# Kernel optimization log

Hardware: AMD Instinct MI355X
Metric: run time of the kernel (lower is better)

Reference implementation:

```python
import jax, jax.numpy as jnp
import numpy as np

N_EMBD = 1024
N_HEAD = 16
HEAD_SIZE = N_EMBD // N_HEAD  # 64

def setup_inputs() -> dict:
    key = jax.random.key(0)
    ks = jax.random.split(key, 6)
    B, T, C, H, S = 2, 2048, N_EMBD, N_HEAD, HEAD_SIZE
    sc = 1.0 / np.sqrt(C)
    x = jax.random.normal(ks[0], (B, T, C), dtype=jnp.float32)
    # stacked per-head projection weights (no bias), [H, C, S]
    Wq = jax.random.normal(ks[1], (H, C, S), dtype=jnp.float32) * sc
    Wk = jax.random.normal(ks[2], (H, C, S), dtype=jnp.float32) * sc
    Wv = jax.random.normal(ks[3], (H, C, S), dtype=jnp.float32) * sc
    Wp = jax.random.normal(ks[4], (C, C), dtype=jnp.float32) * sc
    bp = jax.random.normal(ks[5], (C,), dtype=jnp.float32) * 0.01
    return {"x": x, "Wq": Wq, "Wk": Wk, "Wv": Wv, "Wp": Wp, "bp": bp}

def reference(x, Wq, Wk, Wv, Wp, bp):
    # Eval-mode forward (dropout = identity), default non-flash path.
    B, T, C = x.shape
    H, _, S = Wq.shape
    q = jnp.einsum('btc,hcs->bhts', x, Wq)
    k = jnp.einsum('btc,hcs->bhts', x, Wk)
    v = jnp.einsum('btc,hcs->bhts', x, Wv)
    att = jnp.einsum('bhts,bhus->bhtu', q, k) * (1.0 / np.sqrt(S))
    causal = jnp.tril(jnp.ones((T, T), dtype=bool))
    att = jnp.where(causal[None, None], att, -jnp.inf)
    att = jax.nn.softmax(att, axis=-1)
    y = jnp.einsum('bhtu,bhus->bhts', att, v)
    # concat heads along feature dim (head-major), then output projection
    y = y.transpose(0, 2, 1, 3).reshape(B, T, H * S)
    return y @ Wp.T + bp
```

## Files before the change

kernel.cpp:

```cpp
#include <hip/hip_runtime.h>
#include <hip/hip_bf16.h>
#include <cmath>

typedef __attribute__((ext_vector_type(8))) short bf16x8;
typedef __attribute__((ext_vector_type(4))) float f32x4;
typedef __attribute__((ext_vector_type(16))) float f32x16;

__device__ __forceinline__ unsigned short f2bf(float f) {
    union { float f; unsigned int i; } c; c.f = f;
    unsigned int i = c.i;
    unsigned int r = i + 0x7FFF + ((i >> 16) & 1);
    return (unsigned short)(r >> 16);
}

__device__ __forceinline__ float fast_exp2(float x) {
    float r;
    asm("v_exp_f32 %0, %1" : "=v"(r) : "v"(x));
    return r;
}

__device__ __forceinline__ void gload_lds16(const unsigned short* g, unsigned short* l) {
    __builtin_amdgcn_global_load_lds((const __attribute__((address_space(1))) unsigned int*)g,
                                     (__attribute__((address_space(3))) unsigned int*)l, 16, 0, 0);
}

__device__ __forceinline__ float bperm_f(int srclane, float v) {
    return __int_as_float(__builtin_amdgcn_ds_bpermute(srclane << 2, __float_as_int(v)));
}

__global__ void k_cvt(const float* __restrict__ src, unsigned short* __restrict__ dst, int n4) {
    int i = blockIdx.x * blockDim.x + threadIdx.x;
    if (i < n4) {
        float4 v = reinterpret_cast<const float4*>(src)[i];
        ushort4 o;
        o.x = f2bf(v.x); o.y = f2bf(v.y); o.z = f2bf(v.z); o.w = f2bf(v.w);
        reinterpret_cast<ushort4*>(dst)[i] = o;
    }
}

__global__ void k_cvt_wt(const float* __restrict__ Wq, const float* __restrict__ Wk,
                         const float* __restrict__ Wv, unsigned short* __restrict__ Wt) {
    __shared__ unsigned short lt[64][72];
    int bid = blockIdx.x;
    int ct  = bid & 15;
    int h   = (bid >> 4) & 15;
    int sec = bid >> 8;
    const float* W = (sec == 0) ? Wq : ((sec == 1) ? Wk : Wv);
    int t = threadIdx.x;
    #pragma unroll
    for (int q = 0; q < 4; q++) {
        int id = t + q * 256;
        int c  = id >> 4;
        int s4 = (id & 15) * 4;
        float4 v = *reinterpret_cast<const float4*>(&W[((size_t)(h * 1024) + (ct * 64 + c)) * 64 + s4]);
        lt[s4 + 0][c] = f2bf(v.x);
        lt[s4 + 1][c] = f2bf(v.y);
        lt[s4 + 2][c] = f2bf(v.z);
        lt[s4 + 3][c] = f2bf(v.w);
    }
    __syncthreads();
    #pragma unroll
    for (int q = 0; q < 2; q++) {
        int id = t + q * 256;
        int s  = id >> 3;
        int c8 = (id & 7) * 8;
        bf16x8 val = *reinterpret_cast<const bf16x8*>(&lt[s][c8]);
        int n = sec * 1024 + h * 64 + s;
        *reinterpret_cast<bf16x8*>(&Wt[(size_t)n * 1024 + ct * 64 + c8]) = val;
    }
}

template <int MODE>
__launch_bounds__(256)
__global__ void k_gemm(const unsigned short* __restrict__ A,
                       const unsigned short* __restrict__ Bt,
                       int M, int N, int K,
                       unsigned short* __restrict__ q_nat,
                       unsigned short* __restrict__ k_nat,
                       unsigned short* __restrict__ vT,
                       float* __restrict__ out, const float* __restrict__ bp) {
    __shared__ unsigned short Asm[128][64];
    __shared__ unsigned short Bsm[128][64];
    const int nb = N >> 7;
    int cpx = gridDim.x >> 3;
    int bid = (blockIdx.x & 7) * cpx + (blockIdx.x >> 3);
    int n0 = (bid % nb) << 7;
    int m0 = (bid / nb) << 7;
    int t = threadIdx.x;
    int lane = t & 63, w = t >> 6;
    int wr = w >> 1, wc = w & 1;
    int l15 = lane & 15, lg = lane >> 4;
    int sr = lane >> 3;
    int scol = ((lane & 7) ^ sr) << 3;

    f32x4 acc[4][4];
    #pragma unroll
    for (int i = 0; i < 4; i++)
        #pragma unroll
        for (int j = 0; j < 4; j++) acc[i][j] = (f32x4){0.f, 0.f, 0.f, 0.f};

    for (int kt = 0; kt < K; kt += 64) {
        #pragma unroll
        for (int q = 0; q < 4; q++) {
            int rb = q * 32 + w * 8;
            int row = rb + sr;
            gload_lds16(&A[(size_t)(m0 + row) * K + kt + scol], &Asm[rb][0]);
            gload_lds16(&Bt[(size_t)(n0 + row) * K + kt + scol], &Bsm[rb][0]);
        }
        __syncthreads();
        bf16x8 af[4][2], bfr[4][2];
        int x15 = (l15 & 7) << 3;
        #pragma unroll
        for (int mi = 0; mi < 4; mi++) {
            int row = wr * 64 + mi * 16 + l15;
            af[mi][0] = *reinterpret_cast<const bf16x8*>(&Asm[row][(lg * 8) ^ x15]);
            af[mi][1] = *reinterpret_cast<const bf16x8*>(&Asm[row][(32 + lg * 8) ^ x15]);
        }
        #pragma unroll
        for (int nj = 0; nj < 4; nj++) {
            int row = wc * 64 + nj * 16 + l15;
            bfr[nj][0] = *reinterpret_cast<const bf16x8*>(&Bsm[row][(lg * 8) ^ x15]);
            bfr[nj][1] = *reinterpret_cast<const bf16x8*>(&Bsm[row][(32 + lg * 8) ^ x15]);
        }
        #pragma unroll
        for (int mi = 0; mi < 4; mi++)
            #pragma unroll
            for (int nj = 0; nj < 4; nj++) {
                acc[mi][nj] = __builtin_amdgcn_mfma_f32_16x16x32_bf16(af[mi][0], bfr[nj][0], acc[mi][nj], 0, 0, 0);
                acc[mi][nj] = __builtin_amdgcn_mfma_f32_16x16x32_bf16(af[mi][1], bfr[nj][1], acc[mi][nj], 0, 0, 0);
            }
        __syncthreads();
    }

    #pragma unroll
    for (int mi = 0; mi < 4; mi++) {
        #pragma unroll
        for (int nj = 0; nj < 4; nj++) {
            #pragma unroll
            for (int r = 0; r < 4; r++) {
                int m = m0 + wr * 64 + mi * 16 + lg * 4 + r;
                int n = n0 + wc * 64 + nj * 16 + l15;
                float v = acc[mi][nj][r];
                if (MODE == 0) {
                    int sec = n >> 10;
                    int win = n & 1023;
                    if (sec == 0) {
                        q_nat[(size_t)m * 1024 + win] = f2bf(v * 0.1803368801f);
                    } else if (sec == 1) {
                        k_nat[(size_t)m * 1024 + win] = f2bf(v);
                    } else {
                        int b = m >> 11, tt = m & 2047;
                        int h = win >> 6, s = win & 63;
                        vT[(((size_t)(b * 16 + h)) * 64 + s) * 2048 + tt] = f2bf(v);
                    }
                } else {
                    out[(size_t)m * 1024 + n] = v + bp[n];
                }
            }
        }
    }
}

__launch_bounds__(256, 4)
__global__ void k_attn(const unsigned short* __restrict__ q_nat,
                       const unsigned short* __restrict__ k_nat,
                       const unsigned short* __restrict__ vT,
                       unsigned short* __restrict__ y_bf) {
    __shared__ __align__(16) unsigned short Ks[2][64][64];
    __shared__ __align__(16) unsigned short Vs[2][64][64];
    __shared__ float cm[2][64], cl[2][64];
    const int T = 2048, H = 16;
    int bid = blockIdx.x;
    int bh = bid & 31;
    int qi = 31 - (bid >> 5);
    int h = bh & 15, b = bh >> 4;
    int t = threadIdx.x;
    int lane = t & 63, w = t >> 6;
    int pr = w >> 1, rg = w & 1;
    int l31 = lane & 31, hi = lane >> 5;
    int warp_q0 = qi * 64 + rg * 32;
    int qg = warp_q0 + l31;

    int n0 = (qi >> 1) + 1;
    int nS = pr ? ((qi + 1) >> 1) : n0;

    const unsigned short* kbase = k_nat + (size_t)(b * T) * 1024 + h * 64;
    const unsigned short* vbase = vT + ((size_t)(b * H + h) * 64) * 2048;

    int sxor = ((lane & 7) ^ (lane >> 3)) << 3;

    auto STAGE = [&](int j) {
        #pragma unroll
        for (int r = 0; r < 4; r++) {
            int rb = r * 16 + rg * 8;
            int grow = rb + (lane >> 3);
            gload_lds16(kbase + (size_t)(j * 64 + grow) * 1024 + sxor, &Ks[pr][rb][0]);
            gload_lds16(vbase + (size_t)grow * 2048 + j * 64 + sxor, &Vs[pr][rb][0]);
        }
    };

    bf16x8 qf[4];
    #pragma unroll
    for (int tt = 0; tt < 4; tt++)
        qf[tt] = *reinterpret_cast<const bf16x8*>(
            q_nat + (size_t)(b * T + qg) * 1024 + h * 64 + tt * 16 + hi * 8);

    f32x16 acc0, acc1;
    #pragma unroll
    for (int r = 0; r < 16; r++) { acc0[r] = 0.f; acc1[r] = 0.f; }
    float m = -INFINITY, ell = 0.f;

    for (int i = 0; i < n0; i++) {
        bool act = (i < nS);
        int j = pr + 2 * i;
        if (act) STAGE(j);
        __syncthreads();

        if (act) {
            const char* kb = (const char*)&Ks[pr][0][0];
            const char* vb = (const char*)&Vs[pr][0][0];
            int rsw = (l31 & 7) << 4;

            f32x16 s0, s1;
            #pragma unroll
            for (int r = 0; r < 16; r++) { s0[r] = 0.f; s1[r] = 0.f; }
            __builtin_amdgcn_s_setprio(1);
            #pragma unroll
            for (int tt = 0; tt < 4; tt++) {
                int cb = (tt * 32 + hi * 16) ^ rsw;
                bf16x8 kf0 = *reinterpret_cast<const bf16x8*>(kb + l31 * 128 + cb);
                bf16x8 kf1 = *reinterpret_cast<const bf16x8*>(kb + (32 + l31) * 128 + cb);
                s0 = __builtin_amdgcn_mfma_f32_32x32x16_bf16(kf0, qf[tt], s0, 0, 0, 0);
                s1 = __builtin_amdgcn_mfma_f32_32x32x16_bf16(kf1, qf[tt], s1, 0, 0, 0);
            }
            __builtin_amdgcn_s_setprio(0);

            if (j == qi) {
                #pragma unroll
                for (int r = 0; r < 16; r++) {
                    int kvr = (r & 3) + 8 * (r >> 2) + 4 * hi + j * 64;
                    if (kvr > qg) s0[r] = -INFINITY;
                    if (kvr + 32 > qg) s1[r] = -INFINITY;
                }
            }

            float tmax = -INFINITY;
            #pragma unroll
            for (int r = 0; r < 16; r++) tmax = fmaxf(tmax, fmaxf(s0[r], s1[r]));
            tmax = fmaxf(tmax, __shfl_xor(tmax, 32, 64));

            if (!__all(tmax <= m + 11.5f)) {
                float mn = fmaxf(m, tmax);
                float scl = fast_exp2(m - mn);
                m = mn; ell *= scl;
                #pragma unroll
                for (int r = 0; r < 16; r++) {
                    float sv = bperm_f((r & 3) + 8 * (r >> 2) + 4 * hi, scl);
                    acc0[r] *= sv; acc1[r] *= sv;
                }
            }

            float rs = 0.f;
            #pragma unroll
            for (int r = 0; r < 16; r++) {
                s0[r] = fast_exp2(s0[r] - m); rs += s0[r];
                s1[r] = fast_exp2(s1[r] - m); rs += s1[r];
            }
            rs += __shfl_xor(rs, 32, 64);
            ell += rs;

            unsigned int c[16];
            #pragma unroll
            for (int i2 = 0; i2 < 8; i2++) {
                asm("v_cvt_pk_bf16_f32 %0, %1, %2" : "=v"(c[i2]) : "v"(s0[2 * i2]), "v"(s0[2 * i2 + 1]));
                asm("v_cvt_pk_bf16_f32 %0, %1, %2" : "=v"(c[8 + i2]) : "v"(s1[2 * i2]), "v"(s1[2 * i2 + 1]));
            }
            bf16x8 pa[4];
            #pragma unroll
            for (int ks = 0; ks < 4; ks++) {
                unsigned int clo0 = c[ks * 4 + 0], clo1 = c[ks * 4 + 1];
                unsigned int chi0 = c[ks * 4 + 2], chi1 = c[ks * 4 + 3];
                unsigned int pl0 = (unsigned int)__shfl_xor((int)clo0, 32, 64);
                unsigned int pl1 = (unsigned int)__shfl_xor((int)clo1, 32, 64);
                unsigned int ph0 = (unsigned int)__shfl_xor((int)chi0, 32, 64);
                unsigned int ph1 = (unsigned int)__shfl_xor((int)chi1, 32, 64);
                union { unsigned int u[4]; bf16x8 v; } fr;
                fr.u[0] = hi ? ph0 : clo0;
                fr.u[1] = hi ? ph1 : clo1;
                fr.u[2] = hi ? chi0 : pl0;
                fr.u[3] = hi ? chi1 : pl1;
                pa[ks] = fr.v;
            }

            __builtin_amdgcn_s_setprio(1);
            #pragma unroll
            for (int ks = 0; ks < 4; ks++) {
                int cb = (ks * 32 + hi * 16) ^ rsw;
                bf16x8 v0 = *reinterpret_cast<const bf16x8*>(vb + l31 * 128 + cb);
                bf16x8 v1 = *reinterpret_cast<const bf16x8*>(vb + (32 + l31) * 128 + cb);
                acc0 = __builtin_amdgcn_mfma_f32_32x32x16_bf16(pa[ks], v0, acc0, 0, 0, 0);
                acc1 = __builtin_amdgcn_mfma_f32_32x32x16_bf16(pa[ks], v1, acc1, 0, 0, 0);
            }
            __builtin_amdgcn_s_setprio(0);
        }

        __syncthreads();
    }

    if (hi == 0) { cm[pr][rg * 32 + l31] = m; cl[pr][rg * 32 + l31] = ell; }
    __syncthreads();

    int rowi = rg * 32 + l31;
    float m0v = cm[0][rowi], l0v = cl[0][rowi];
    float m1v = cm[1][rowi], l1v = cl[1][rowi];
    float mSt = fmaxf(m0v, m1v);
    float w0 = (m0v > -1e30f) ? fast_exp2(m0v - mSt) : 0.f;
    float w1 = (m1v > -1e30f) ? fast_exp2(m1v - mSt) : 0.f;
    float denom = 1.f / (l0v * w0 + l1v * w1);
    float myw = pr ? w1 : w0;

    float* Ocomb = (float*)&Ks[0][0][0];
    if (pr == 1) {
        #pragma unroll
        for (int r = 0; r < 16; r++) {
            int qr = (r & 3) + 8 * (r >> 2) + 4 * hi;
            float sB = bperm_f(qr, myw);
            Ocomb[(rg * 32 + qr) * 64 + l31] = acc0[r] * sB;
            Ocomb[(rg * 32 + qr) * 64 + 32 + l31] = acc1[r] * sB;
        }
    }
    __syncthreads();
    if (pr == 0) {
        #pragma unroll
        for (int r = 0; r < 16; r++) {
            int qr = (r & 3) + 8 * (r >> 2) + 4 * hi;
            float sA = bperm_f(qr, myw);
            float dv = bperm_f(qr, denom);
            float o0 = acc0[r] * sA + Ocomb[(rg * 32 + qr) * 64 + l31];
            float o1 = acc1[r] * sA + Ocomb[(rg * 32 + qr) * 64 + 32 + l31];
            size_t row = (size_t)(b * T + warp_q0 + qr) * 1024 + h * 64;
            y_bf[row + l31] = f2bf(o0 * dv);
            y_bf[row + 32 + l31] = f2bf(o1 * dv);
        }
    }
}

extern "C" void kernel_launch(void* const* d_in, const int* in_sizes, int n_in,
                              void* d_out, int out_size, void* d_ws, size_t ws_size,
                              hipStream_t stream) {
    const float* x  = (const float*)d_in[0];
    const float* Wq = (const float*)d_in[1];
    const float* Wk = (const float*)d_in[2];
    const float* Wv = (const float*)d_in[3];
    const float* Wp = (const float*)d_in[4];
    const float* bp = (const float*)d_in[5];
    float* out = (float*)d_out;

    char* ws = (char*)d_ws;
    unsigned short* x_bf  = (unsigned short*)(ws);
    unsigned short* Wt    = (unsigned short*)(ws + ((size_t)8  << 20));
    unsigned short* Wp_bf = (unsigned short*)(ws + ((size_t)14 << 20));
    unsigned short* q_nat = (unsigned short*)(ws + ((size_t)16 << 20));
    unsigned short* k_nat = (unsigned short*)(ws + ((size_t)24 << 20));
    unsigned short* vT    = (unsigned short*)(ws + ((size_t)32 << 20));
    unsigned short* y_bf  = (unsigned short*)(ws + ((size_t)40 << 20));

    k_cvt<<<4096, 256, 0, stream>>>(x, x_bf, 4194304 / 4);
    k_cvt<<<1024, 256, 0, stream>>>(Wp, Wp_bf, 1048576 / 4);
    k_cvt_wt<<<768, 256, 0, stream>>>(Wq, Wk, Wv, Wt);
    k_gemm<0><<<24 * 32, 256, 0, stream>>>(x_bf, Wt, 4096, 3072, 1024,
                                           q_nat, k_nat, vT, nullptr, nullptr);
    k_attn<<<1024, 256, 0, stream>>>(q_nat, k_nat, vT, y_bf);
    k_gemm<1><<<8 * 32, 256, 0, stream>>>(y_bf, Wp_bf, 4096, 1024, 1024,
                                          nullptr, nullptr, nullptr, out, bp);
}
```

Measured before the change: 118.2 us.

## Double-buffer GEMM LDS tiles and compute V projection transposed for coalesced vT writes

The GEMM main loop now double-buffers the A/B LDS tiles, prefetching the next K-slice while running MFMAs on the current one. It uses explicit waitcnt, barriers and setprio around the MFMA block. The V projection is split into its own GEMM launch that computes Wv^T·x^T, so vT is written with contiguous time-major stores instead of strided scatters. The Q scale is folded into the weight conversion. The cost is twice the LDS per block and one extra kernel launch.

Measured after the change: 119.5 us. Within noise of the previous version (+1.1%).

```diff
diff --git a/kernel.cpp b/kernel.cpp
--- a/kernel.cpp
+++ b/kernel.cpp
@@ -46,6 +46,7 @@
     int h   = (bid >> 4) & 15;
     int sec = bid >> 8;
     const float* W = (sec == 0) ? Wq : ((sec == 1) ? Wk : Wv);
+    float sc = (sec == 0) ? 0.1803368801f : 1.0f;
     int t = threadIdx.x;
     #pragma unroll
     for (int q = 0; q < 4; q++) {
@@ -53,10 +54,10 @@
         int c  = id >> 4;
         int s4 = (id & 15) * 4;
         float4 v = *reinterpret_cast<const float4*>(&W[((size_t)(h * 1024) + (ct * 64 + c)) * 64 + s4]);
-        lt[s4 + 0][c] = f2bf(v.x);
-        lt[s4 + 1][c] = f2bf(v.y);
-        lt[s4 + 2][c] = f2bf(v.z);
-        lt[s4 + 3][c] = f2bf(v.w);
+        lt[s4 + 0][c] = f2bf(v.x * sc);
+        lt[s4 + 1][c] = f2bf(v.y * sc);
+        lt[s4 + 2][c] = f2bf(v.z * sc);
+        lt[s4 + 3][c] = f2bf(v.w * sc);
     }
     __syncthreads();
     #pragma unroll
@@ -71,7 +72,7 @@
 }
 
 template <int MODE>
-__launch_bounds__(256)
+__launch_bounds__(256, 2)
 __global__ void k_gemm(const unsigned short* __restrict__ A,
                        const unsigned short* __restrict__ Bt,
                        int M, int N, int K,
@@ -79,8 +80,8 @@
                        unsigned short* __restrict__ k_nat,
                        unsigned short* __restrict__ vT,
                        float* __restrict__ out, const float* __restrict__ bp) {
-    __shared__ unsigned short Asm[128][64];
-    __shared__ unsigned short Bsm[128][64];
+    __shared__ unsigned short Asm[2][128][64];
+    __shared__ unsigned short Bsm[2][128][64];
     const int nb = N >> 7;
     int cpx = gridDim.x >> 3;
     int bid = (blockIdx.x & 7) * cpx + (blockIdx.x >> 3);
@@ -99,29 +100,42 @@
         #pragma unroll
         for (int j = 0; j < 4; j++) acc[i][j] = (f32x4){0.f, 0.f, 0.f, 0.f};
 
-    for (int kt = 0; kt < K; kt += 64) {
+    auto STAGE = [&](int kt, int buf) {
         #pragma unroll
         for (int q = 0; q < 4; q++) {
             int rb = q * 32 + w * 8;
             int row = rb + sr;
-            gload_lds16(&A[(size_t)(m0 + row) * K + kt + scol], &Asm[rb][0]);
-            gload_lds16(&Bt[(size_t)(n0 + row) * K + kt + scol], &Bsm[rb][0]);
-        }
-        __syncthreads();
+            gload_lds16(&A[(size_t)(m0 + row) * K + kt + scol], &Asm[buf][rb][0]);
+            gload_lds16(&Bt[(size_t)(n0 + row) * K + kt + scol], &Bsm[buf][rb][0]);
+        }
+    };
+
+    const int NT = K >> 6;
+    STAGE(0, 0);
+    asm volatile("s_waitcnt vmcnt(0)" ::: "memory");
+    __builtin_amdgcn_s_barrier();
+    int cur = 0;
+
+    for (int tt = 0; tt < NT; tt++) {
+        if (tt + 1 < NT) STAGE((tt + 1) << 6, cur ^ 1);
+
         bf16x8 af[4][2], bfr[4][2];
         int x15 = (l15 & 7) << 3;
         #pragma unroll
         for (int mi = 0; mi < 4; mi++) {
             int row = wr * 64 + mi * 16 + l15;
-            af[mi][0] = *reinterpret_cast<const bf16x8*>(&Asm[row][(lg * 8) ^ x15]);
-            af[mi][1] = *reinterpret_cast<const bf16x8*>(&Asm[row][(32 + lg * 8) ^ x15]);
+            af[mi][0] = *reinterpret_cast<const bf16x8*>(&Asm[cur][row][(lg * 8) ^ x15]);
+            af[mi][1] = *reinterpret_cast<const bf16x8*>(&Asm[cur][row][(32 + lg * 8) ^ x15]);
         }
         #pragma unroll
         for (int nj = 0; nj < 4; nj++) {
             int row = wc * 64 + nj * 16 + l15;
-            bfr[nj][0] = *reinterpret_cast<const bf16x8*>(&Bsm[row][(lg * 8) ^ x15]);
-            bfr[nj][1] = *reinterpret_cast<const bf16x8*>(&Bsm[row][(32 + lg * 8) ^ x15]);
-        }
+            bfr[nj][0] = *reinterpret_cast<const bf16x8*>(&Bsm[cur][row][(lg * 8) ^ x15]);
+            bfr[nj][1] = *reinterpret_cast<const bf16x8*>(&Bsm[cur][row][(32 + lg * 8) ^ x15]);
+        }
+        asm volatile("s_waitcnt lgkmcnt(0)" ::: "memory");
+        __builtin_amdgcn_sched_barrier(0);
+        __builtin_amdgcn_s_setprio(1);
         #pragma unroll
         for (int mi = 0; mi < 4; mi++)
             #pragma unroll
@@ -129,9 +143,16 @@
                 acc[mi][nj] = __builtin_amdgcn_mfma_f32_16x16x32_bf16(af[mi][0], bfr[nj][0], acc[mi][nj], 0, 0, 0);
                 acc[mi][nj] = __builtin_amdgcn_mfma_f32_16x16x32_bf16(af[mi][1], bfr[nj][1], acc[mi][nj], 0, 0, 0);
             }
-        __syncthreads();
-    }
-
+        __builtin_amdgcn_s_setprio(0);
+
+        asm volatile("s_waitcnt vmcnt(0)" ::: "memory");
+        __builtin_amdgcn_s_barrier();
+        cur ^= 1;
+    }
+
+    unsigned short* qkdst = nullptr;
+    int noff = 0;
+    if (MODE == 0) { qkdst = (n0 < 1024) ? q_nat : k_nat; noff = (n0 < 1024) ? 0 : 1024; }
     #pragma unroll
     for (int mi = 0; mi < 4; mi++) {
         #pragma unroll
@@ -142,17 +163,11 @@
                 int n = n0 + wc * 64 + nj * 16 + l15;
                 float v = acc[mi][nj][r];
                 if (MODE == 0) {
-                    int sec = n >> 10;
-                    int win = n & 1023;
-                    if (sec == 0) {
-                        q_nat[(size_t)m * 1024 + win] = f2bf(v * 0.1803368801f);
-                    } else if (sec == 1) {
-                        k_nat[(size_t)m * 1024 + win] = f2bf(v);
-                    } else {
-                        int b = m >> 11, tt = m & 2047;
-                        int h = win >> 6, s = win & 63;
-                        vT[(((size_t)(b * 16 + h)) * 64 + s) * 2048 + tt] = f2bf(v);
-                    }
+                    qkdst[(size_t)m * 1024 + (n - noff)] = f2bf(v);
+                } else if (MODE == 2) {
+                    int bb = n >> 11, ttn = n & 2047;
+                    int hh = m >> 6, ss = m & 63;
+                    vT[(((size_t)(bb * 16 + hh)) * 64 + ss) * 2048 + ttn] = f2bf(v);
                 } else {
                     out[(size_t)m * 1024 + n] = v + bp[n];
                 }
@@ -368,9 +383,11 @@
     k_cvt<<<4096, 256, 0, stream>>>(x, x_bf, 4194304 / 4);
     k_cvt<<<1024, 256, 0, stream>>>(Wp, Wp_bf, 1048576 / 4);
     k_cvt_wt<<<768, 256, 0, stream>>>(Wq, Wk, Wv, Wt);
-    k_gemm<0><<<24 * 32, 256, 0, stream>>>(x_bf, Wt, 4096, 3072, 1024,
-                                           q_nat, k_nat, vT, nullptr, nullptr);
+    k_gemm<0><<<32 * 16, 256, 0, stream>>>(x_bf, Wt, 4096, 2048, 1024,
+                                           q_nat, k_nat, nullptr, nullptr, nullptr);
+    k_gemm<2><<<8 * 32, 256, 0, stream>>>(Wt + (size_t)2048 * 1024, x_bf, 1024, 4096, 1024,
+                                          nullptr, nullptr, vT, nullptr, nullptr);
     k_attn<<<1024, 256, 0, stream>>>(q_nat, k_nat, vT, y_bf);
-    k_gemm<1><<<8 * 32, 256, 0, stream>>>(y_bf, Wp_bf, 4096, 1024, 1024,
+    k_gemm<1><<<32 * 8, 256, 0, stream>>>(y_bf, Wp_bf, 4096, 1024, 1024,
                                           nullptr, nullptr, nullptr, out, bp);
 }
```
